# Kernel optimization log

Hardware: AMD Instinct MI355X
Metric: run time of the kernel (lower is better)

## Reference

```python
import jax, jax.numpy as jnp
import numpy as np
from jax import lax

B = 32      # point clouds per batch
P = 1024    # points per cloud (equal-sized, contiguous in batch vector)
K = 20      # kNN neighbors (includes self, as in PyG knn)
N = B * P


def _w(key, fan_in, fan_out):
    return jax.random.normal(key, (fan_in, fan_out), dtype=jnp.float32) / np.sqrt(fan_in)


def setup_inputs() -> dict:
    key = jax.random.key(0)
    ks = jax.random.split(key, 12)
    return {
        "pos": jax.random.normal(ks[0], (N, 3), dtype=jnp.float32),
        "batch": jnp.repeat(jnp.arange(B, dtype=jnp.int32), P),
        # conv1 MLP([6,64,64]): Linear(6,64)+BN+ReLU, Linear(64,64) plain
        "conv1_W1": _w(ks[1], 6, 64),
        "conv1_b1": jnp.zeros((64,), jnp.float32),
        "conv1_bn_scale": jnp.ones((64,), jnp.float32),   # BN eval folded affine
        "conv1_bn_bias": jnp.zeros((64,), jnp.float32),
        "conv1_W2": _w(ks[2], 64, 64),
        "conv1_b2": jnp.zeros((64,), jnp.float32),
        # conv2 MLP([128,128]): single plain Linear(128,128)
        "conv2_W": _w(ks[3], 128, 128),
        "conv2_b": jnp.zeros((128,), jnp.float32),
        # lin: Linear(64+128, 128)
        "lin_W": _w(ks[4], 192, 128),
        "lin_b": jnp.zeros((128,), jnp.float32),
    }


def _edge_conv(x, mlp_fn):
    # x: [B, P, d]. Dynamic kNN in feature space per cloud, edge MLP, max-aggregate.
    sq = jnp.sum(x * x, axis=-1)                                  # [B,P]
    dist = sq[:, :, None] - 2.0 * jnp.einsum('bpd,bqd->bpq', x, x) + sq[:, None, :]
    _, idx = lax.top_k(-dist, K)                                  # [B,P,K] nearest (incl. self)
    x_j = jax.vmap(lambda xb, ib: xb[ib])(x, idx)                 # [B,P,K,d] gather neighbors
    x_i = jnp.broadcast_to(x[:, :, None, :], x_j.shape)
    e = jnp.concatenate([x_i, x_j - x_i], axis=-1)                # [B,P,K,2d]
    return jnp.max(mlp_fn(e), axis=2)                             # max aggregation -> [B,P,out]


def reference(pos, batch, conv1_W1, conv1_b1, conv1_bn_scale, conv1_bn_bias,
              conv1_W2, conv1_b2, conv2_W, conv2_b, lin_W, lin_b):
    x = pos.reshape(B, P, 3)

    def mlp1(e):
        h = e @ conv1_W1 + conv1_b1
        h = jax.nn.relu(h * conv1_bn_scale + conv1_bn_bias)       # BN(eval) + ReLU
        return h @ conv1_W2 + conv1_b2                            # plain last layer

    def mlp2(e):
        return e @ conv2_W + conv2_b                              # plain single layer

    x1 = _edge_conv(x, mlp1)                                      # [B,P,64]
    x2 = _edge_conv(x1, mlp2)                                     # [B,P,128]
    h = jnp.concatenate([x1, x2], axis=-1) @ lin_W + lin_b        # [B,P,128]
    # global_max_pool over each cloud via batch ids
    out = jax.ops.segment_max(h.reshape(N, 128), batch, num_segments=B)
    return out                                                    # [B,128]
```

## Files before the change

### kernel.cpp

```cpp
#include <hip/hip_runtime.h>
#include <math.h>

#define NPTS 32768
#define NB 32
#define PP 1024
#define KK 20

using bf16x8 = __attribute__((ext_vector_type(8))) short;
using f32x4 = __attribute__((ext_vector_type(4))) float;

constexpr size_t OFF_X1 = 0;
constexpr size_t OFF_IDX = OFF_X1 + (size_t)NPTS * 64 * 4;
constexpr size_t OFF_U = OFF_IDX + (size_t)NPTS * KK * 4;
constexpr size_t OFF_V = OFF_U + (size_t)NPTS * 128 * 4;
constexpr size_t OFF_X2 = OFF_V + (size_t)NPTS * 128 * 4;
constexpr size_t OFF_H = OFF_X2 + (size_t)NPTS * 128 * 4;
constexpr size_t OFF_PART = OFF_H + (size_t)NPTS * 128 * 4;
constexpr size_t OFF_SQN = OFF_PART + (size_t)32 * 8 * 128 * 4;

__device__ __forceinline__ void topk_insert(unsigned (&l)[KK], unsigned key) {
#pragma unroll
  for (int j = KK - 1; j >= 1; --j) {
    unsigned r;
    asm("v_med3_u32 %0, %1, %2, %3" : "=v"(r) : "v"(key), "v"(l[j - 1]), "v"(l[j]));
    l[j] = r;
  }
  l[0] = key < l[0] ? key : l[0];
}

__device__ __forceinline__ unsigned pack_key(float dist, int q) {
  return (__float_as_uint(dist) & 0xFFFFFC00u) | (unsigned)q;
}

__device__ __forceinline__ void split_bf16(float x, short& hi, short& lo) {
  unsigned u = __float_as_uint(x);
  hi = (short)(u >> 16);
  float fh = __uint_as_float(u & 0xFFFF0000u);
  float r = x - fh;
  lo = (short)(__float_as_uint(r) >> 16);
}

template <int S>
__global__ __launch_bounds__(256, 4) void knn_topk3(const float* __restrict__ x,
                                                    unsigned* __restrict__ pk) {
  constexpr int CH = PP / S;
  __shared__ __align__(16) float xs[1024];
  __shared__ __align__(16) float ys[1024];
  __shared__ __align__(16) float zs[1024];
  int bx = blockIdx.x;
  int s = bx % S;
  int tile = (bx / S) % (PP / 256);
  int b = bx / (S * (PP / 256));
  int tid = threadIdx.x;
  const float* xb = x + (size_t)b * PP * 3;

  for (int t = tid; t < 768; t += 256) {
    float4 v = ((const float4*)xb)[t];
    int e = 4 * t;
    float vals[4] = {v.x, v.y, v.z, v.w};
#pragma unroll
    for (int j = 0; j < 4; ++j) {
      int p = (e + j) / 3, d = (e + j) % 3;
      if (d == 0) xs[p] = vals[j];
      else if (d == 1) ys[p] = vals[j];
      else zs[p] = vals[j];
    }
  }
  __syncthreads();

  int i = tile * 256 + tid;
  float xi0 = xs[i], xi1 = ys[i], xi2 = zs[i];

  unsigned l[KK];
#pragma unroll
  for (int j = 0; j < KK; ++j) l[j] = 0xFFFFFFFFu;

  int q0 = s * CH;
  float4 qx = *(const float4*)&xs[q0];
  float4 qy = *(const float4*)&ys[q0];
  float4 qz = *(const float4*)&zs[q0];
  for (int c = 0; c < CH; c += 4) {
    int qm = (q0 + c + 4) & 1023;
    float4 nqx = *(const float4*)&xs[qm];
    float4 nqy = *(const float4*)&ys[qm];
    float4 nqz = *(const float4*)&zs[qm];
    float cx[4] = {qx.x, qx.y, qx.z, qx.w};
    float cy[4] = {qy.x, qy.y, qy.z, qy.w};
    float cz[4] = {qz.x, qz.y, qz.z, qz.w};
#pragma unroll
    for (int j = 0; j < 4; ++j) {
      float d0 = xi0 - cx[j], d1 = xi1 - cy[j], d2 = xi2 - cz[j];
      float dist = fmaf(d0, d0, fmaf(d1, d1, d2 * d2));
      topk_insert(l, pack_key(dist, q0 + c + j));
    }
    qx = nqx; qy = nqy; qz = nqz;
  }
  size_t base = ((size_t)b * PP + i) * S + s;
#pragma unroll
  for (int j = 0; j < KK; ++j) pk[base * KK + j] = l[j];
}

template <int S>
__global__ __launch_bounds__(256) void knn_merge(const unsigned* __restrict__ pk,
                                                 int* __restrict__ idx_out) {
  int p = blockIdx.x * 256 + threadIdx.x;
  const unsigned* g = pk + (size_t)p * S * KK;
  unsigned l[KK];
#pragma unroll
  for (int j = 0; j < KK; ++j) l[j] = g[j];
  for (int s = 1; s < S; ++s) {
    const unsigned* gs = g + s * KK;
    for (int j = 0; j < KK; ++j) {
      unsigned key = gs[j];
      if (key >= l[KK - 1]) break;
      topk_insert(l, key);
    }
  }
#pragma unroll
  for (int j = 0; j < KK; ++j) idx_out[(size_t)p * KK + j] = (int)(l[j] & 1023u);
}

__global__ __launch_bounds__(256) void precompute1(const float* __restrict__ pos,
                                                   const float* __restrict__ W1,
                                                   const float* __restrict__ b1,
                                                   float* __restrict__ u1,
                                                   float* __restrict__ v1) {
  int gid = blockIdx.x * 256 + threadIdx.x;
  int i = gid >> 6, c = gid & 63;
  float p0 = pos[(size_t)i * 3 + 0], p1 = pos[(size_t)i * 3 + 1], p2 = pos[(size_t)i * 3 + 2];
  float a0 = W1[0 * 64 + c], a1 = W1[1 * 64 + c], a2 = W1[2 * 64 + c];
  float g0 = W1[3 * 64 + c], g1 = W1[4 * 64 + c], g2 = W1[5 * 64 + c];
  float v = fmaf(p0, g0, fmaf(p1, g1, p2 * g2));
  float u = b1[c];
  u = fmaf(p0, a0 - g0, u);
  u = fmaf(p1, a1 - g1, u);
  u = fmaf(p2, a2 - g2, u);
  u1[gid] = u;
  v1[gid] = v;
}

__global__ __launch_bounds__(256) void edge_conv1_mfma(
    const float* __restrict__ u1, const float* __restrict__ v1,
    const int* __restrict__ idx, const float* __restrict__ W2,
    const float* __restrict__ scale, const float* __restrict__ bias,
    const float* __restrict__ b2,
    short* __restrict__ x1hl, float* __restrict__ sqn) {
  __shared__ int jt[32 * KK];
  __shared__ float mxs[32 * 68];
  int tid = threadIdx.x;
  int p0 = blockIdx.x * 32;
  int b = p0 >> 10;
  for (int t = tid; t < 32 * KK; t += 256)
    jt[t] = (b << 10) + idx[(size_t)(p0 + t / KK) * KK + t % KK];
  int w = tid >> 6, l = tid & 63, quad = l >> 4, lm = l & 15;
  int group = w >> 1, khalf = w & 1;
  int kq = quad * 8;
  bf16x8 Bh[4][2], Bl[4][2];
#pragma unroll
  for (int nt = 0; nt < 4; ++nt) {
#pragma unroll
    for (int ks = 0; ks < 2; ++ks) {
#pragma unroll
      for (int jj = 0; jj < 8; ++jj) {
        float wv = W2[(size_t)(ks * 32 + kq + jj) * 64 + nt * 16 + lm];
        short hi, lo;
        split_bf16(wv, hi, lo);
        Bh[nt][ks][jj] = hi;
        Bl[nt][ks][jj] = lo;
      }
    }
  }
  int myp = group * 16 + lm;
  const float* urow = u1 + (size_t)(p0 + myp) * 64;
  float up[2][8], sc[2][8];
#pragma unroll
  for (int ks = 0; ks < 2; ++ks) {
    int koff = ks * 32 + kq;
    float4 ua = *(const float4*)(urow + koff);
    float4 ub = *(const float4*)(urow + koff + 4);
    float4 sa = *(const float4*)(scale + koff);
    float4 sb = *(const float4*)(scale + koff + 4);
    float4 ca = *(const float4*)(bias + koff);
    float4 cb4 = *(const float4*)(bias + koff + 4);
    sc[ks][0] = sa.x; sc[ks][1] = sa.y; sc[ks][2] = sa.z; sc[ks][3] = sa.w;
    sc[ks][4] = sb.x; sc[ks][5] = sb.y; sc[ks][6] = sb.z; sc[ks][7] = sb.w;
    up[ks][0] = fmaf(ua.x, sa.x, ca.x);
    up[ks][1] = fmaf(ua.y, sa.y, ca.y);
    up[ks][2] = fmaf(ua.z, sa.z, ca.z);
    up[ks][3] = fmaf(ua.w, sa.w, ca.w);
    up[ks][4] = fmaf(ub.x, sb.x, cb4.x);
    up[ks][5] = fmaf(ub.y, sb.y, cb4.y);
    up[ks][6] = fmaf(ub.z, sb.z, cb4.z);
    up[ks][7] = fmaf(ub.w, sb.w, cb4.w);
  }
  float b2v[4];
#pragma unroll
  for (int nt = 0; nt < 4; ++nt) b2v[nt] = b2[nt * 16 + lm];
  __syncthreads();

  f32x4 mx[4];
#pragma unroll
  for (int nt = 0; nt < 4; ++nt)
    mx[nt] = (f32x4){-__builtin_inff(), -__builtin_inff(), -__builtin_inff(), -__builtin_inff()};

  for (int k = khalf * 10; k < khalf * 10 + 10; ++k) {
    int j = jt[myp * KK + k];
    const float* vrow = v1 + (size_t)j * 64;
    f32x4 acc[4];
#pragma unroll
    for (int nt = 0; nt < 4; ++nt) acc[nt] = (f32x4){0.f, 0.f, 0.f, 0.f};
#pragma unroll
    for (int ks = 0; ks < 2; ++ks) {
      int koff = ks * 32 + kq;
      float4 va = *(const float4*)(vrow + koff);
      float4 vb = *(const float4*)(vrow + koff + 4);
      float hv[8];
      hv[0] = fmaxf(fmaf(va.x, sc[ks][0], up[ks][0]), 0.f);
      hv[1] = fmaxf(fmaf(va.y, sc[ks][1], up[ks][1]), 0.f);
      hv[2] = fmaxf(fmaf(va.z, sc[ks][2], up[ks][2]), 0.f);
      hv[3] = fmaxf(fmaf(va.w, sc[ks][3], up[ks][3]), 0.f);
      hv[4] = fmaxf(fmaf(vb.x, sc[ks][4], up[ks][4]), 0.f);
      hv[5] = fmaxf(fmaf(vb.y, sc[ks][5], up[ks][5]), 0.f);
      hv[6] = fmaxf(fmaf(vb.z, sc[ks][6], up[ks][6]), 0.f);
      hv[7] = fmaxf(fmaf(vb.w, sc[ks][7], up[ks][7]), 0.f);
      bf16x8 Ah, Al;
#pragma unroll
      for (int jj = 0; jj < 8; ++jj) {
        short hi, lo;
        split_bf16(hv[jj], hi, lo);
        Ah[jj] = hi;
        Al[jj] = lo;
      }
#pragma unroll
      for (int nt = 0; nt < 4; ++nt) {
        acc[nt] = __builtin_amdgcn_mfma_f32_16x16x32_bf16(Ah, Bh[nt][ks], acc[nt], 0, 0, 0);
        acc[nt] = __builtin_amdgcn_mfma_f32_16x16x32_bf16(Al, Bh[nt][ks], acc[nt], 0, 0, 0);
        acc[nt] = __builtin_amdgcn_mfma_f32_16x16x32_bf16(Ah, Bl[nt][ks], acc[nt], 0, 0, 0);
      }
    }
#pragma unroll
    for (int nt = 0; nt < 4; ++nt) {
#pragma unroll
      for (int r = 0; r < 4; ++r) mx[nt][r] = fmaxf(mx[nt][r], acc[nt][r]);
    }
  }
  if (khalf == 1) {
#pragma unroll
    for (int nt = 0; nt < 4; ++nt)
#pragma unroll
      for (int r = 0; r < 4; ++r)
        mxs[(group * 16 + quad * 4 + r) * 68 + nt * 16 + lm] = mx[nt][r];
  }
  __syncthreads();
  if (khalf == 0) {
#pragma unroll
    for (int nt = 0; nt < 4; ++nt) {
#pragma unroll
      for (int r = 0; r < 4; ++r) {
        int p = group * 16 + quad * 4 + r;
        int c = nt * 16 + lm;
        float m = fmaxf(mx[nt][r], mxs[p * 68 + c]) + b2v[nt];
        short hi, lo;
        split_bf16(m, hi, lo);
        size_t gi = (size_t)(p0 + p) * 128 + c;
        x1hl[gi] = hi;
        x1hl[gi + 64] = lo;
        mxs[p * 68 + c] = m;
      }
    }
  }
  __syncthreads();
  if (tid < 32) {
    float ss = 0.f;
    for (int c = 0; c < 64; ++c) {
      float v = mxs[tid * 68 + c];
      ss = fmaf(v, v, ss);
    }
    sqn[p0 + tid] = ss;
  }
}

__global__ __launch_bounds__(256, 4) void knn2_mfma(const short* __restrict__ x1hl,
                                                    const float* __restrict__ sqn,
                                                    unsigned* __restrict__ pk) {
  constexpr int TS = 72;
  __shared__ float sqs[512];
  __shared__ __align__(16) short tileH[2][64 * TS];
  __shared__ __align__(16) short tileL[2][64 * TS];
  int bx = blockIdx.x;
  int s = bx & 1;
  int pb = bx >> 1;
  int p0 = pb * 64;
  int b = p0 >> 10;
  int tid = threadIdx.x;
  for (int t = tid; t < 512; t += 256) sqs[t] = sqn[(size_t)b * PP + s * 512 + t];
  int w = tid >> 6, l = tid & 63, quad = l >> 4, lm = l & 15;
  size_t gi = (size_t)p0 + w * 16 + lm;
  const short* brow = x1hl + gi * 128 + quad * 8;
  bf16x8 Bh0 = *(const bf16x8*)(brow);
  bf16x8 Bl0 = *(const bf16x8*)(brow + 64);
  bf16x8 Bh1 = *(const bf16x8*)(brow + 32);
  bf16x8 Bl1 = *(const bf16x8*)(brow + 96);
  float sqi = sqn[gi];

  unsigned la[KK], lc[KK];
#pragma unroll
  for (int j = 0; j < KK; ++j) { la[j] = 0xFFFFFFFFu; lc[j] = 0xFFFFFFFFu; }

  int rr = tid & 63, seg = tid >> 6;
  const short* srcbase = x1hl + ((size_t)b * PP + s * 512 + rr) * 128 + seg * 32;
  {
    bf16x8 r0 = *(const bf16x8*)(srcbase);
    bf16x8 r1 = *(const bf16x8*)(srcbase + 8);
    bf16x8 r2 = *(const bf16x8*)(srcbase + 16);
    bf16x8 r3 = *(const bf16x8*)(srcbase + 24);
    short* dst = ((seg < 2) ? tileH[0] : tileL[0]) + rr * TS + (seg & 1) * 32;
    *(bf16x8*)(dst) = r0;
    *(bf16x8*)(dst + 8) = r1;
    *(bf16x8*)(dst + 16) = r2;
    *(bf16x8*)(dst + 24) = r3;
  }
  __syncthreads();

  for (int tile = 0; tile < 8; ++tile) {
    int buf = tile & 1;
    bf16x8 r0, r1, r2, r3;
    if (tile < 7) {
      const short* src = srcbase + (size_t)(tile + 1) * 64 * 128;
      r0 = *(const bf16x8*)(src);
      r1 = *(const bf16x8*)(src + 8);
      r2 = *(const bf16x8*)(src + 16);
      r3 = *(const bf16x8*)(src + 24);
    }
#pragma unroll
    for (int it = 0; it < 4; ++it) {
      int row = it * 16 + lm;
      const short* aH = tileH[buf] + row * TS + quad * 8;
      const short* aL = tileL[buf] + row * TS + quad * 8;
      bf16x8 Ah0 = *(const bf16x8*)(aH);
      bf16x8 Ah1 = *(const bf16x8*)(aH + 32);
      bf16x8 Al0 = *(const bf16x8*)(aL);
      bf16x8 Al1 = *(const bf16x8*)(aL + 32);

      f32x4 acc = (f32x4){0.f, 0.f, 0.f, 0.f};
      acc = __builtin_amdgcn_mfma_f32_16x16x32_bf16(Ah0, Bh0, acc, 0, 0, 0);
      acc = __builtin_amdgcn_mfma_f32_16x16x32_bf16(Al0, Bh0, acc, 0, 0, 0);
      acc = __builtin_amdgcn_mfma_f32_16x16x32_bf16(Ah0, Bl0, acc, 0, 0, 0);
      acc = __builtin_amdgcn_mfma_f32_16x16x32_bf16(Ah1, Bh1, acc, 0, 0, 0);
      acc = __builtin_amdgcn_mfma_f32_16x16x32_bf16(Al1, Bh1, acc, 0, 0, 0);
      acc = __builtin_amdgcn_mfma_f32_16x16x32_bf16(Ah1, Bl1, acc, 0, 0, 0);

      int qloc = tile * 64 + it * 16 + quad * 4;
      int qg = s * 512 + qloc;
      float d0 = fmaxf(0.f, fmaf(-2.f, acc[0], sqi + sqs[qloc + 0]));
      float d2 = fmaxf(0.f, fmaf(-2.f, acc[2], sqi + sqs[qloc + 2]));
      topk_insert(la, pack_key(d0, qg + 0));
      topk_insert(lc, pack_key(d2, qg + 2));
      float d1 = fmaxf(0.f, fmaf(-2.f, acc[1], sqi + sqs[qloc + 1]));
      float d3 = fmaxf(0.f, fmaf(-2.f, acc[3], sqi + sqs[qloc + 3]));
      topk_insert(la, pack_key(d1, qg + 1));
      topk_insert(lc, pack_key(d3, qg + 3));
    }
    if (tile < 7) {
      __syncthreads();
      short* dst = ((seg < 2) ? tileH[buf ^ 1] : tileL[buf ^ 1]) + rr * TS + (seg & 1) * 32;
      *(bf16x8*)(dst) = r0;
      *(bf16x8*)(dst + 8) = r1;
      *(bf16x8*)(dst + 16) = r2;
      *(bf16x8*)(dst + 24) = r3;
      __syncthreads();
    }
  }
  for (int j = 0; j < KK; ++j) {
    unsigned key = lc[j];
    if (key >= la[KK - 1]) break;
    topk_insert(la, key);
  }
  unsigned sub = (unsigned)(s * 4 + quad);
  unsigned* dst = pk + ((size_t)gi * 8 + sub) * KK;
#pragma unroll
  for (int j = 0; j < KK; ++j) dst[j] = la[j];
}

__global__ __launch_bounds__(256) void pre2_mfma(const short* __restrict__ x1hl,
                                                 const float* __restrict__ cW,
                                                 const float* __restrict__ cb,
                                                 float* __restrict__ u2,
                                                 float* __restrict__ v2) {
  constexpr int BS = 72;
  __shared__ short Bh[128 * BS];
  __shared__ short Bl[128 * BS];
  int tid = threadIdx.x;
  int nh = blockIdx.x & 1;
  int p0 = (blockIdx.x >> 1) * 64;
  for (int t = tid; t < 64 * 128; t += 256) {
    int k = t >> 7, n = t & 127;
    float wb_ = cW[(size_t)(64 + k) * 128 + n];
    float wv = nh ? wb_ : (cW[(size_t)k * 128 + n] - wb_);
    short hi, lo;
    split_bf16(wv, hi, lo);
    Bh[n * BS + k] = hi;
    Bl[n * BS + k] = lo;
  }
  __syncthreads();
  int w = tid >> 6, l = tid & 63, quad = l >> 4, lm = l & 15;
  int row = p0 + w * 16 + lm;
  f32x4 acc[8];
#pragma unroll
  for (int nt = 0; nt < 8; ++nt) acc[nt] = (f32x4){0.f, 0.f, 0.f, 0.f};
#pragma unroll
  for (int ks = 0; ks < 2; ++ks) {
    int kb = ks * 32 + quad * 8;
    bf16x8 Ah = *(const bf16x8*)(x1hl + (size_t)row * 128 + kb);
    bf16x8 Al = *(const bf16x8*)(x1hl + (size_t)row * 128 + 64 + kb);
#pragma unroll
    for (int nt = 0; nt < 8; ++nt) {
      bf16x8 Wh = *(const bf16x8*)(Bh + (nt * 16 + lm) * BS + kb);
      bf16x8 Wl = *(const bf16x8*)(Bl + (nt * 16 + lm) * BS + kb);
      acc[nt] = __builtin_amdgcn_mfma_f32_16x16x32_bf16(Ah, Wh, acc[nt], 0, 0, 0);
      acc[nt] = __builtin_amdgcn_mfma_f32_16x16x32_bf16(Al, Wh, acc[nt], 0, 0, 0);
      acc[nt] = __builtin_amdgcn_mfma_f32_16x16x32_bf16(Ah, Wl, acc[nt], 0, 0, 0);
    }
  }
  float* out = nh ? v2 : u2;
  int prow = p0 + w * 16 + quad * 4;
#pragma unroll
  for (int nt = 0; nt < 8; ++nt) {
    int col = nt * 16 + lm;
    float bias = nh ? 0.f : cb[col];
#pragma unroll
    for (int r = 0; r < 4; ++r)
      out[(size_t)(prow + r) * 128 + col] = acc[nt][r] + bias;
  }
}

__global__ __launch_bounds__(256) void gathermax2(const float* __restrict__ u2,
                                                  const float* __restrict__ v2,
                                                  const int* __restrict__ idx,
                                                  short* __restrict__ x2hl) {
  int gid = blockIdx.x * 256 + threadIdx.x;
  int i = gid >> 7, c = gid & 127;
  int b = i >> 10;
  const int* myidx = idx + (size_t)i * KK;
  float m = -__builtin_inff();
  for (int k = 0; k < KK; ++k) {
    int j = (b << 10) + myidx[k];
    m = fmaxf(m, v2[(size_t)j * 128 + c]);
  }
  float x = u2[gid] + m;
  short hi, lo;
  split_bf16(x, hi, lo);
  x2hl[(size_t)i * 256 + c] = hi;
  x2hl[(size_t)i * 256 + 128 + c] = lo;
}

__global__ __launch_bounds__(256) void lin_mfma(const short* __restrict__ x1hl,
                                                const short* __restrict__ x2hl,
                                                const float* __restrict__ LW,
                                                const float* __restrict__ lb,
                                                float* __restrict__ h) {
  constexpr int BS = 200;
  __shared__ short Bh[64 * BS];
  __shared__ short Bl[64 * BS];
  int tid = threadIdx.x;
  int nh = blockIdx.x & 1;
  int p0 = (blockIdx.x >> 1) * 64;
  for (int t = tid; t < 192 * 64; t += 256) {
    int k = t >> 6, n = t & 63;
    float wv = LW[(size_t)k * 128 + nh * 64 + n];
    short hi, lo;
    split_bf16(wv, hi, lo);
    Bh[n * BS + k] = hi;
    Bl[n * BS + k] = lo;
  }
  __syncthreads();
  int w = tid >> 6, l = tid & 63, quad = l >> 4, lm = l & 15;
  int row = p0 + w * 16 + lm;
  f32x4 acc[4];
#pragma unroll
  for (int nt = 0; nt < 4; ++nt) acc[nt] = (f32x4){0.f, 0.f, 0.f, 0.f};
#pragma unroll
  for (int ks = 0; ks < 6; ++ks) {
    int kb = ks * 32 + quad * 8;
    bf16x8 Ah, Al;
    if (ks < 2) {
      Ah = *(const bf16x8*)(x1hl + (size_t)row * 128 + kb);
      Al = *(const bf16x8*)(x1hl + (size_t)row * 128 + 64 + kb);
    } else {
      Ah = *(const bf16x8*)(x2hl + (size_t)row * 256 + (kb - 64));
      Al = *(const bf16x8*)(x2hl + (size_t)row * 256 + 128 + (kb - 64));
    }
#pragma unroll
    for (int nt = 0; nt < 4; ++nt) {
      bf16x8 Wh = *(const bf16x8*)(Bh + (nt * 16 + lm) * BS + kb);
      bf16x8 Wl = *(const bf16x8*)(Bl + (nt * 16 + lm) * BS + kb);
      acc[nt] = __builtin_amdgcn_mfma_f32_16x16x32_bf16(Ah, Wh, acc[nt], 0, 0, 0);
      acc[nt] = __builtin_amdgcn_mfma_f32_16x16x32_bf16(Al, Wh, acc[nt], 0, 0, 0);
      acc[nt] = __builtin_amdgcn_mfma_f32_16x16x32_bf16(Ah, Wl, acc[nt], 0, 0, 0);
    }
  }
  int prow = p0 + w * 16 + quad * 4;
#pragma unroll
  for (int nt = 0; nt < 4; ++nt) {
    int col = nh * 64 + nt * 16 + lm;
    float bias = lb[col];
#pragma unroll
    for (int r = 0; r < 4; ++r)
      h[(size_t)(prow + r) * 128 + col] = acc[nt][r] + bias;
  }
}

__global__ __launch_bounds__(128) void segmax_a(const float* __restrict__ h,
                                                float* __restrict__ part) {
  int b = blockIdx.x >> 3, chunk = blockIdx.x & 7;
  int c = threadIdx.x;
  float m = -__builtin_inff();
  for (int p = 0; p < 128; ++p) {
    size_t i = (size_t)b * PP + chunk * 128 + p;
    m = fmaxf(m, h[i * 128 + c]);
  }
  part[(size_t)blockIdx.x * 128 + c] = m;
}

__global__ __launch_bounds__(128) void segmax_b(const float* __restrict__ part,
                                                float* __restrict__ out) {
  int b = blockIdx.x;
  int c = threadIdx.x;
  float m = -__builtin_inff();
  for (int k = 0; k < 8; ++k) m = fmaxf(m, part[((size_t)b * 8 + k) * 128 + c]);
  out[(size_t)b * 128 + c] = m;
}

extern "C" void kernel_launch(void* const* d_in, const int* in_sizes, int n_in,
                              void* d_out, int out_size, void* d_ws, size_t ws_size,
                              hipStream_t stream) {
  const float* pos = (const float*)d_in[0];
  const float* W1 = (const float*)d_in[2];
  const float* b1 = (const float*)d_in[3];
  const float* bn_s = (const float*)d_in[4];
  const float* bn_b = (const float*)d_in[5];
  const float* W2 = (const float*)d_in[6];
  const float* b2 = (const float*)d_in[7];
  const float* cW = (const float*)d_in[8];
  const float* cb = (const float*)d_in[9];
  const float* LW = (const float*)d_in[10];
  const float* lb = (const float*)d_in[11];
  float* out = (float*)d_out;

  char* ws = (char*)d_ws;
  short* x1hl = (short*)(ws + OFF_X1);
  int* idx = (int*)(ws + OFF_IDX);
  float* u1 = (float*)(ws + OFF_U);
  float* v1 = (float*)(ws + OFF_V);
  float* u2 = (float*)(ws + OFF_U);
  float* v2 = (float*)(ws + OFF_V);
  short* x2hl = (short*)(ws + OFF_X2);
  float* hbuf = (float*)(ws + OFF_H);
  float* part = (float*)(ws + OFF_PART);
  float* sqn = (float*)(ws + OFF_SQN);
  unsigned* pk = (unsigned*)(ws + OFF_U);

  knn_topk3<8><<<NB * 4 * 8, 256, 0, stream>>>(pos, pk);
  knn_merge<8><<<NPTS / 256, 256, 0, stream>>>(pk, idx);
  precompute1<<<NPTS * 64 / 256, 256, 0, stream>>>(pos, W1, b1, u1, v1);
  edge_conv1_mfma<<<NPTS / 32, 256, 0, stream>>>(u1, v1, idx, W2, bn_s, bn_b, b2,
                                                 x1hl, sqn);
  knn2_mfma<<<NPTS / 64 * 2, 256, 0, stream>>>(x1hl, sqn, pk);
  knn_merge<8><<<NPTS / 256, 256, 0, stream>>>(pk, idx);
  pre2_mfma<<<NPTS / 64 * 2, 256, 0, stream>>>(x1hl, cW, cb, u2, v2);
  gathermax2<<<NPTS * 128 / 256, 256, 0, stream>>>(u2, v2, idx, x2hl);
  lin_mfma<<<NPTS / 64 * 2, 256, 0, stream>>>(x1hl, x2hl, LW, lb, hbuf);
  segmax_a<<<NB * 8, 128, 0, stream>>>(hbuf, part);
  segmax_b<<<NB, 128, 0, stream>>>(part, out);
}
```

Baseline: 335.2 us.

## Split kNN top-k into two interleaved lists and spread edge_conv1 neighbors across 4 waves

In knn_topk3 each thread now keeps two independent top-K lists, fed alternately by candidates, and merges them at the end. This breaks the serial dependency chain of med3 insertions so more instructions can be in flight, at the cost of more registers and a merge pass. In edge_conv1_mfma each block now handles 16 points with all 4 waves splitting the 20 neighbors (5 each). A shared-memory 4-way max reduction and twice as many blocks replace the previous 2-way split over 32 points.

```diff
diff --git a/kernel.cpp b/kernel.cpp
--- a/kernel.cpp
+++ b/kernel.cpp
@@ -71,9 +71,9 @@
   int i = tile * 256 + tid;
   float xi0 = xs[i], xi1 = ys[i], xi2 = zs[i];
 
-  unsigned l[KK];
-#pragma unroll
-  for (int j = 0; j < KK; ++j) l[j] = 0xFFFFFFFFu;
+  unsigned la[KK], lb_[KK];
+#pragma unroll
+  for (int j = 0; j < KK; ++j) { la[j] = 0xFFFFFFFFu; lb_[j] = 0xFFFFFFFFu; }
 
   int q0 = s * CH;
   float4 qx = *(const float4*)&xs[q0];
@@ -87,17 +87,28 @@
     float cx[4] = {qx.x, qx.y, qx.z, qx.w};
     float cy[4] = {qy.x, qy.y, qy.z, qy.w};
     float cz[4] = {qz.x, qz.y, qz.z, qz.w};
-#pragma unroll
-    for (int j = 0; j < 4; ++j) {
-      float d0 = xi0 - cx[j], d1 = xi1 - cy[j], d2 = xi2 - cz[j];
-      float dist = fmaf(d0, d0, fmaf(d1, d1, d2 * d2));
-      topk_insert(l, pack_key(dist, q0 + c + j));
+    {
+      float d0 = xi0 - cx[0], d1 = xi1 - cy[0], d2 = xi2 - cz[0];
+      float e0 = xi0 - cx[2], e1 = xi1 - cy[2], e2 = xi2 - cz[2];
+      topk_insert(la, pack_key(fmaf(d0, d0, fmaf(d1, d1, d2 * d2)), q0 + c + 0));
+      topk_insert(lb_, pack_key(fmaf(e0, e0, fmaf(e1, e1, e2 * e2)), q0 + c + 2));
+    }
+    {
+      float d0 = xi0 - cx[1], d1 = xi1 - cy[1], d2 = xi2 - cz[1];
+      float e0 = xi0 - cx[3], e1 = xi1 - cy[3], e2 = xi2 - cz[3];
+      topk_insert(la, pack_key(fmaf(d0, d0, fmaf(d1, d1, d2 * d2)), q0 + c + 1));
+      topk_insert(lb_, pack_key(fmaf(e0, e0, fmaf(e1, e1, e2 * e2)), q0 + c + 3));
     }
     qx = nqx; qy = nqy; qz = nqz;
   }
+  for (int j = 0; j < KK; ++j) {
+    unsigned key = lb_[j];
+    if (key >= la[KK - 1]) break;
+    topk_insert(la, key);
+  }
   size_t base = ((size_t)b * PP + i) * S + s;
 #pragma unroll
-  for (int j = 0; j < KK; ++j) pk[base * KK + j] = l[j];
+  for (int j = 0; j < KK; ++j) pk[base * KK + j] = la[j];
 }
 
 template <int S>
@@ -145,15 +156,14 @@
     const float* __restrict__ scale, const float* __restrict__ bias,
     const float* __restrict__ b2,
     short* __restrict__ x1hl, float* __restrict__ sqn) {
-  __shared__ int jt[32 * KK];
-  __shared__ float mxs[32 * 68];
+  __shared__ int jt[16 * KK];
+  __shared__ float mxs[4][16 * 68];
   int tid = threadIdx.x;
-  int p0 = blockIdx.x * 32;
+  int p0 = blockIdx.x * 16;
   int b = p0 >> 10;
-  for (int t = tid; t < 32 * KK; t += 256)
+  for (int t = tid; t < 16 * KK; t += 256)
     jt[t] = (b << 10) + idx[(size_t)(p0 + t / KK) * KK + t % KK];
   int w = tid >> 6, l = tid & 63, quad = l >> 4, lm = l & 15;
-  int group = w >> 1, khalf = w & 1;
   int kq = quad * 8;
   bf16x8 Bh[4][2], Bl[4][2];
 #pragma unroll
@@ -170,8 +180,7 @@
       }
     }
   }
-  int myp = group * 16 + lm;
-  const float* urow = u1 + (size_t)(p0 + myp) * 64;
+  const float* urow = u1 + (size_t)(p0 + lm) * 64;
   float up[2][8], sc[2][8];
 #pragma unroll
   for (int ks = 0; ks < 2; ++ks) {
@@ -193,9 +202,6 @@
     up[ks][6] = fmaf(ub.z, sb.z, cb4.z);
     up[ks][7] = fmaf(ub.w, sb.w, cb4.w);
   }
-  float b2v[4];
-#pragma unroll
-  for (int nt = 0; nt < 4; ++nt) b2v[nt] = b2[nt * 16 + lm];
   __syncthreads();
 
   f32x4 mx[4];
@@ -203,8 +209,8 @@
   for (int nt = 0; nt < 4; ++nt)
     mx[nt] = (f32x4){-__builtin_inff(), -__builtin_inff(), -__builtin_inff(), -__builtin_inff()};
 
-  for (int k = khalf * 10; k < khalf * 10 + 10; ++k) {
-    int j = jt[myp * KK + k];
+  for (int k = w * 5; k < w * 5 + 5; ++k) {
+    int j = jt[lm * KK + k];
     const float* vrow = v1 + (size_t)j * 64;
     f32x4 acc[4];
 #pragma unroll
@@ -244,36 +250,28 @@
       for (int r = 0; r < 4; ++r) mx[nt][r] = fmaxf(mx[nt][r], acc[nt][r]);
     }
   }
-  if (khalf == 1) {
-#pragma unroll
-    for (int nt = 0; nt < 4; ++nt)
-#pragma unroll
-      for (int r = 0; r < 4; ++r)
-        mxs[(group * 16 + quad * 4 + r) * 68 + nt * 16 + lm] = mx[nt][r];
-  }
-  __syncthreads();
-  if (khalf == 0) {
-#pragma unroll
-    for (int nt = 0; nt < 4; ++nt) {
-#pragma unroll
-      for (int r = 0; r < 4; ++r) {
-        int p = group * 16 + quad * 4 + r;
-        int c = nt * 16 + lm;
-        float m = fmaxf(mx[nt][r], mxs[p * 68 + c]) + b2v[nt];
-        short hi, lo;
-        split_bf16(m, hi, lo);
-        size_t gi = (size_t)(p0 + p) * 128 + c;
-        x1hl[gi] = hi;
-        x1hl[gi + 64] = lo;
-        mxs[p * 68 + c] = m;
-      }
-    }
-  }
-  __syncthreads();
-  if (tid < 32) {
+#pragma unroll
+  for (int nt = 0; nt < 4; ++nt)
+#pragma unroll
+    for (int r = 0; r < 4; ++r)
+      mxs[w][(quad * 4 + r) * 68 + nt * 16 + lm] = mx[nt][r];
+  __syncthreads();
+  for (int o = tid; o < 1024; o += 256) {
+    int p = o >> 6, c = o & 63;
+    float m = fmaxf(fmaxf(mxs[0][p * 68 + c], mxs[1][p * 68 + c]),
+                    fmaxf(mxs[2][p * 68 + c], mxs[3][p * 68 + c])) + b2[c];
+    short hi, lo;
+    split_bf16(m, hi, lo);
+    size_t gi = (size_t)(p0 + p) * 128 + c;
+    x1hl[gi] = hi;
+    x1hl[gi + 64] = lo;
+    mxs[0][p * 68 + c] = m;
+  }
+  __syncthreads();
+  if (tid < 16) {
     float ss = 0.f;
     for (int c = 0; c < 64; ++c) {
-      float v = mxs[tid * 68 + c];
+      float v = mxs[0][tid * 68 + c];
       ss = fmaf(v, v, ss);
     }
     sqn[p0 + tid] = ss;
@@ -563,7 +561,7 @@
   knn_topk3<8><<<NB * 4 * 8, 256, 0, stream>>>(pos, pk);
   knn_merge<8><<<NPTS / 256, 256, 0, stream>>>(pk, idx);
   precompute1<<<NPTS * 64 / 256, 256, 0, stream>>>(pos, W1, b1, u1, v1);
-  edge_conv1_mfma<<<NPTS / 32, 256, 0, stream>>>(u1, v1, idx, W2, bn_s, bn_b, b2,
+  edge_conv1_mfma<<<NPTS / 16, 256, 0, stream>>>(u1, v1, idx, W2, bn_s, bn_b, b2,
                                                  x1hl, sqn);
   knn2_mfma<<<NPTS / 64 * 2, 256, 0, stream>>>(x1hl, sqn, pk);
   knn_merge<8><<<NPTS / 256, 256, 0, stream>>>(pk, idx);
```

Result: slower. 351.9 us (+5.0%).

## Dual top-k lists in knn scan and fuse segment max into lin GEMM

Applied to the files above, without the earlier changes.

The first-layer kNN scan now keeps two independent top-k insertion lists, fed alternately by the candidate points. This breaks the serial dependency chain of v_med3 insertions, and the two lists are merged at the end. Separately, the lin MFMA kernel now reduces its tile to per-block column maxima in shared memory and writes partials directly, which removes the 16MB h buffer write and the segmax_a kernel. The cost is doubled register use for the top-k lists, which risks lower occupancy or spilling, plus an extra merge pass.

```diff
diff --git a/kernel.cpp b/kernel.cpp
--- a/kernel.cpp
+++ b/kernel.cpp
@@ -71,9 +71,9 @@
   int i = tile * 256 + tid;
   float xi0 = xs[i], xi1 = ys[i], xi2 = zs[i];
 
-  unsigned l[KK];
-#pragma unroll
-  for (int j = 0; j < KK; ++j) l[j] = 0xFFFFFFFFu;
+  unsigned la[KK], lb_[KK];
+#pragma unroll
+  for (int j = 0; j < KK; ++j) { la[j] = 0xFFFFFFFFu; lb_[j] = 0xFFFFFFFFu; }
 
   int q0 = s * CH;
   float4 qx = *(const float4*)&xs[q0];
@@ -87,17 +87,28 @@
     float cx[4] = {qx.x, qx.y, qx.z, qx.w};
     float cy[4] = {qy.x, qy.y, qy.z, qy.w};
     float cz[4] = {qz.x, qz.y, qz.z, qz.w};
-#pragma unroll
-    for (int j = 0; j < 4; ++j) {
-      float d0 = xi0 - cx[j], d1 = xi1 - cy[j], d2 = xi2 - cz[j];
-      float dist = fmaf(d0, d0, fmaf(d1, d1, d2 * d2));
-      topk_insert(l, pack_key(dist, q0 + c + j));
+    {
+      float d0 = xi0 - cx[0], d1 = xi1 - cy[0], d2 = xi2 - cz[0];
+      float e0 = xi0 - cx[2], e1 = xi1 - cy[2], e2 = xi2 - cz[2];
+      topk_insert(la, pack_key(fmaf(d0, d0, fmaf(d1, d1, d2 * d2)), q0 + c + 0));
+      topk_insert(lb_, pack_key(fmaf(e0, e0, fmaf(e1, e1, e2 * e2)), q0 + c + 2));
+    }
+    {
+      float d0 = xi0 - cx[1], d1 = xi1 - cy[1], d2 = xi2 - cz[1];
+      float e0 = xi0 - cx[3], e1 = xi1 - cy[3], e2 = xi2 - cz[3];
+      topk_insert(la, pack_key(fmaf(d0, d0, fmaf(d1, d1, d2 * d2)), q0 + c + 1));
+      topk_insert(lb_, pack_key(fmaf(e0, e0, fmaf(e1, e1, e2 * e2)), q0 + c + 3));
     }
     qx = nqx; qy = nqy; qz = nqz;
   }
+  for (int j = 0; j < KK; ++j) {
+    unsigned key = lb_[j];
+    if (key >= la[KK - 1]) break;
+    topk_insert(la, key);
+  }
   size_t base = ((size_t)b * PP + i) * S + s;
 #pragma unroll
-  for (int j = 0; j < KK; ++j) pk[base * KK + j] = l[j];
+  for (int j = 0; j < KK; ++j) pk[base * KK + j] = la[j];
 }
 
 template <int S>
@@ -458,10 +469,11 @@
                                                 const short* __restrict__ x2hl,
                                                 const float* __restrict__ LW,
                                                 const float* __restrict__ lb,
-                                                float* __restrict__ h) {
+                                                float* __restrict__ part) {
   constexpr int BS = 200;
   __shared__ short Bh[64 * BS];
   __shared__ short Bl[64 * BS];
+  __shared__ float red[16][68];
   int tid = threadIdx.x;
   int nh = blockIdx.x & 1;
   int p0 = (blockIdx.x >> 1) * 64;
@@ -499,36 +511,32 @@
       acc[nt] = __builtin_amdgcn_mfma_f32_16x16x32_bf16(Ah, Wl, acc[nt], 0, 0, 0);
     }
   }
-  int prow = p0 + w * 16 + quad * 4;
+  int g = w * 4 + quad;
 #pragma unroll
   for (int nt = 0; nt < 4; ++nt) {
     int col = nh * 64 + nt * 16 + lm;
-    float bias = lb[col];
-#pragma unroll
-    for (int r = 0; r < 4; ++r)
-      h[(size_t)(prow + r) * 128 + col] = acc[nt][r] + bias;
-  }
-}
-
-__global__ __launch_bounds__(128) void segmax_a(const float* __restrict__ h,
-                                                float* __restrict__ part) {
-  int b = blockIdx.x >> 3, chunk = blockIdx.x & 7;
-  int c = threadIdx.x;
-  float m = -__builtin_inff();
-  for (int p = 0; p < 128; ++p) {
-    size_t i = (size_t)b * PP + chunk * 128 + p;
-    m = fmaxf(m, h[i * 128 + c]);
-  }
-  part[(size_t)blockIdx.x * 128 + c] = m;
+    float m = fmaxf(fmaxf(acc[nt][0], acc[nt][1]), fmaxf(acc[nt][2], acc[nt][3])) + lb[col];
+    red[g][nt * 16 + lm] = m;
+  }
+  __syncthreads();
+  if (tid < 64) {
+    float m = red[0][tid];
+#pragma unroll
+    for (int gg = 1; gg < 16; ++gg) m = fmaxf(m, red[gg][tid]);
+    int b = p0 >> 10, chunk = (p0 >> 6) & 15;
+    part[(((size_t)b * 16 + chunk) * 2 + nh) * 64 + tid] = m;
+  }
 }
 
 __global__ __launch_bounds__(128) void segmax_b(const float* __restrict__ part,
                                                 float* __restrict__ out) {
   int b = blockIdx.x;
-  int c = threadIdx.x;
+  int c0 = threadIdx.x;
+  int nh = c0 >> 6, c = c0 & 63;
   float m = -__builtin_inff();
-  for (int k = 0; k < 8; ++k) m = fmaxf(m, part[((size_t)b * 8 + k) * 128 + c]);
-  out[(size_t)b * 128 + c] = m;
+  for (int ch = 0; ch < 16; ++ch)
+    m = fmaxf(m, part[(((size_t)b * 16 + ch) * 2 + nh) * 64 + c]);
+  out[(size_t)b * 128 + c0] = m;
 }
 
 extern "C" void kernel_launch(void* const* d_in, const int* in_sizes, int n_in,
@@ -555,8 +563,7 @@
   float* u2 = (float*)(ws + OFF_U);
   float* v2 = (float*)(ws + OFF_V);
   short* x2hl = (short*)(ws + OFF_X2);
-  float* hbuf = (float*)(ws + OFF_H);
-  float* part = (float*)(ws + OFF_PART);
+  float* part = (float*)(ws + OFF_H);
   float* sqn = (float*)(ws + OFF_SQN);
   unsigned* pk = (unsigned*)(ws + OFF_U);
 
@@ -569,7 +576,6 @@
   knn_merge<8><<<NPTS / 256, 256, 0, stream>>>(pk, idx);
   pre2_mfma<<<NPTS / 64 * 2, 256, 0, stream>>>(x1hl, cW, cb, u2, v2);
   gathermax2<<<NPTS * 128 / 256, 256, 0, stream>>>(u2, v2, idx, x2hl);
-  lin_mfma<<<NPTS / 64 * 2, 256, 0, stream>>>(x1hl, x2hl, LW, lb, hbuf);
-  segmax_a<<<NB * 8, 128, 0, stream>>>(hbuf, part);
+  lin_mfma<<<NPTS / 64 * 2, 256, 0, stream>>>(x1hl, x2hl, LW, lb, part);
   segmax_b<<<NB, 128, 0, stream>>>(part, out);
 }
```

Measured after the change: 315.9 us, median of 3. -5.7%, faster.
